# Performance work log

Hardware: AMD Instinct MI355X
Metric: run time of the kernel (lower is better)

The kernel has to match this reference:

```python
import jax, jax.numpy as jnp
import numpy as np

B, V, FIN, H = 200, 40, 16, 128
NSW = 12          # switch edges
NE = 40           # regular edges
M = NE + NSW      # 52 total edges
MLP_HID = 1024
OUT = M + V + NSW # 104


def _build_graph():
    rng = np.random.default_rng(0)
    pairs = set()
    while len(pairs) < M:
        i, j = map(int, rng.integers(0, V, 2))
        if i < j:
            pairs.add((i, j))
    pairs = sorted(pairs)
    reg = np.array(pairs[:NE], np.int64)   # (NE,2)
    sw = np.array(pairs[NE:], np.int64)    # (NSW,2) row-major sorted, matches torch.nonzero order
    edges = np.concatenate([reg, sw], 0)   # switch edges last, matching graph_topo layout
    A = np.zeros((V, M), np.float32)
    A[edges[:, 0], np.arange(M)] = 1.0
    A[edges[:, 1], np.arange(M)] = -1.0
    return reg, sw, A


def setup_inputs():
    key = jax.random.key(0)
    ks = jax.random.split(key, 16)
    reg, sw, A = _build_graph()
    ei = jnp.broadcast_to(jnp.asarray(reg.T)[None], (B, 2, NE))
    si = jnp.broadcast_to(jnp.asarray(sw.T)[None], (B, 2, NSW))

    def w(k, shp, fan):
        return jax.random.normal(k, shp, jnp.float32) / np.sqrt(fan)

    return {
        'x_mod': jax.random.normal(ks[0], (B, V, FIN), jnp.float32),
        'ei': ei, 'si': si, 'A_inc': jnp.asarray(A),
        'embed': w(ks[1], (2, FIN), 1.0),
        'WU0': w(ks[2], (FIN, H), FIN), 'WV0': w(ks[3], (FIN, H), FIN),
        'WA0': w(ks[4], (FIN, H), FIN), 'WB0': w(ks[5], (FIN, H), FIN),
        'WC0': w(ks[6], (FIN, H), FIN),
        'WU1': w(ks[7], (H, H), H), 'WV1': w(ks[8], (H, H), H),
        'WA1': w(ks[9], (H, H), H), 'WB1': w(ks[10], (H, H), H),
        'WC1': w(ks[11], (H, H), H),
        'W1': w(ks[12], ((NSW + V) * H, MLP_HID), (NSW + V) * H),
        'b1': jnp.zeros((MLP_HID,), jnp.float32),
        'W2': w(ks[13], (MLP_HID, OUT), MLP_HID),
        'b2': jnp.zeros((OUT,), jnp.float32),
    }


def _layer(x, s, adj, smask, WU, WV, WA, WB, WC, residual):
    Ux = x @ WU
    Vx = x @ WV
    # gate features over dense VxV switch grid: e_ij = A s_ij + B x_i + C x_j
    e = jnp.einsum('bijf,fh->bijh', s, WA) + (x @ WB)[:, :, None, :] + (x @ WC)[:, None, :, :]
    gates = jax.nn.sigmoid(e) * smask[..., None]
    msg_edges = jnp.einsum('bij,bjh->bih', adj, Vx)   # regular-edge aggregation
    msg_sw = jnp.einsum('bijh,bjh->bih', gates, Vx)   # gated switch aggregation
    xh = jax.nn.relu(Ux + msg_edges + msg_sw)
    sh = jax.nn.relu(e)
    if residual:
        xh = x + xh
        sh = s + sh
    return xh, sh


def reference(x_mod, ei, si, A_inc, embed, WU0, WV0, WA0, WB0, WC0,
              WU1, WV1, WA1, WB1, WC1, W1, b1, W2, b2):
    i_sw, j_sw = si[0, 0], si[0, 1]   # switch indices (shared across batch)
    i_e, j_e = ei[0, 0], ei[0, 1]
    S = jnp.zeros((V, V), bool).at[i_sw, j_sw].set(True)   # upper-tri switch mask
    smask = jnp.broadcast_to(S, (B, V, V)).astype(x_mod.dtype)
    s0 = embed[S.astype(jnp.int32)]                        # (V,V,FIN) edge embedding
    s = jnp.broadcast_to(s0[None], (B, V, V, FIN))
    adj1 = jnp.zeros((V, V), x_mod.dtype).at[i_e, j_e].set(1.0)
    adj = jnp.broadcast_to((adj1 + adj1.T)[None], (B, V, V))
    x, s = _layer(x_mod, s, adj, smask, WU0, WV0, WA0, WB0, WC0, residual=False)
    x, s = _layer(x, s, adj, smask, WU1, WV1, WA1, WB1, WC1, residual=True)
    switches = s[:, i_sw, j_sw, :]                         # (B,NSW,H) irregular gather (torch.nonzero path)
    mlp_in = jnp.concatenate([switches.reshape(B, -1), x.reshape(B, -1)], axis=1)
    out = jax.nn.relu(mlp_in @ W1 + b1) @ W2 + b2          # (B,OUT)
    p_switch = jax.nn.sigmoid(out[:, -NSW:])
    graph_topo = jnp.ones((B, M), out.dtype).at[:, M - NSW:].set(p_switch)
    v = out[:, M:M + V].at[:, 0].set(1.0)
    p_fc = graph_topo * out[:, :M]
    q_fc = graph_topo * (v @ A_inc)                        # per-edge voltage difference flow
    pg = x_mod[:, :, 0] + jnp.einsum('vm,bm->bv', A_inc, p_fc)  # power balance completion
    qg = x_mod[:, :, 1] + jnp.einsum('vm,bm->bv', A_inc, q_fc)
    z = jnp.concatenate([p_fc, v, graph_topo], axis=1)     # (B, 2M+V)
    zc = jnp.concatenate([q_fc, pg, qg], axis=1)           # (B, M+2V)
    return z, zc
```

## Files before the change

kernel.cpp:

```cpp
#include <hip/hip_runtime.h>
#include <math.h>

#define B       200
#define V       40
#define FIN     16
#define H       128
#define NSW     12
#define NE      40
#define M       52
#define MLP_HID 1024
#define OUTD    104
#define MLP_IN  6656
#define ZDIM    144
#define ZCDIM   132
#define NCH     13
#define X1LD    136
#define MAXD    16

typedef __attribute__((ext_vector_type(8))) short bf16x8;
typedef __attribute__((ext_vector_type(4))) float f32x4;

__device__ __forceinline__ float sigmoidf(float x) {
    return 1.0f / (1.0f + expf(-x));
}
__device__ __forceinline__ unsigned short f2b(float x) {
    unsigned int u = __float_as_uint(x);
    u += 0x7fffu + ((u >> 16) & 1u);
    return (unsigned short)(u >> 16);
}
__device__ __forceinline__ float b2f(unsigned short s) {
    return __uint_as_float(((unsigned int)s) << 16);
}

__global__ __launch_bounds__(256) void k_prep(
        const float* __restrict__ WU0, const float* __restrict__ WV0,
        const float* __restrict__ WB0, const float* __restrict__ WC0,
        const float* __restrict__ WU1, const float* __restrict__ WV1,
        const float* __restrict__ WB1, const float* __restrict__ WC1,
        const float* __restrict__ WA1, const float* __restrict__ W2,
        unsigned short* __restrict__ W0t, unsigned short* __restrict__ Wt640,
        unsigned short* __restrict__ W2t) {
    int bx = blockIdx.x, tid = threadIdx.x;
    if (bx < 64) {
        int o0 = bx * 2048 + tid * 8;
#pragma unroll
        for (int i = 0; i < 8; ++i) {
            int o = o0 + i; int col = o >> 10, k = o & 1023;
            W2t[o] = (col < OUTD) ? f2b(W2[(size_t)k * OUTD + col]) : (unsigned short)0;
        }
    } else if (bx < 104) {
        int o0 = (bx - 64) * 2048 + tid * 8;
#pragma unroll
        for (int i = 0; i < 8; ++i) {
            int o = o0 + i; int col = o >> 7, f = o & 127;
            int m = col >> 7, hh = col & 127;
            const float* Ws = (m == 0) ? WU1 : (m == 1) ? WV1 : (m == 2) ? WB1
                            : (m == 3) ? WC1 : WA1;
            Wt640[o] = f2b(Ws[f * H + hh]);
        }
    } else {
        int o0 = (bx - 104) * 2048 + tid * 8;
#pragma unroll
        for (int i = 0; i < 8; ++i) {
            int o = o0 + i; int col = o >> 5, k = o & 31;
            int m = col >> 7, hh = col & 127;
            const float* Ws = (m == 0) ? WU0 : (m == 1) ? WV0 : (m == 2) ? WB0 : WC0;
            W0t[o] = (k < FIN) ? f2b(Ws[k * H + hh]) : (unsigned short)0;
        }
    }
}

__global__ __launch_bounds__(512) void k_gnn(const float* __restrict__ x,
        const int* __restrict__ ei, const int* __restrict__ si,
        const float* __restrict__ embed, const float* __restrict__ WA0,
        const unsigned short* __restrict__ W0t,
        const unsigned short* __restrict__ Wt640,
        unsigned short* __restrict__ Abf) {
    int b = blockIdx.x, tid = threadIdx.x;
    __shared__ unsigned short xb[48 * 40];
    __shared__ unsigned short uvbc[V * 512];
    __shared__ unsigned short x1l[64 * X1LD];
    __shared__ float gL[NSW * H];
    __shared__ float sA1l[NSW * H];
    __shared__ int   nbr[V][MAXD];
    __shared__ int   deg[V];

    int h = tid & 127, sub = tid >> 7;
    int lane = tid & 63, wv = tid >> 6;
    int lr = lane & 15, lk = lane >> 4;
    int n0w = wv * 64;

    for (int o = tid; o < 48 * 32; o += 512) {
        int r = o >> 5, k = o & 31;
        float v = (r < V && k < FIN) ? x[(size_t)b * V * FIN + r * FIN + k] : 0.f;
        xb[r * 40 + k] = f2b(v);
    }
    if (tid < V) deg[tid] = 0;
    for (int o = tid; o < 12 * 128; o += 512) {
        int rr = o >> 7;
        int row = (rr < 8) ? 40 + rr : 60 + (rr - 8);
        x1l[row * X1LD + (o & 127)] = 0;
    }
    __syncthreads();

    if (tid < NE) {
        int i = ei[tid], j = ei[NE + tid];
        int p = atomicAdd(&deg[i], 1); if (p < MAXD) nbr[i][p] = j;
        int q = atomicAdd(&deg[j], 1); if (q < MAXD) nbr[j][q] = i;
    } else if (tid < NE + NSW) {
        int k = tid - NE;
        int i = si[k], j = si[NSW + k];
        int p = atomicAdd(&deg[i], 1); if (p < MAXD) nbr[i][p] = j | ((k + 1) << 8);
    }
    {
        f32x4 acc[3][4];
#pragma unroll
        for (int rf = 0; rf < 3; ++rf)
#pragma unroll
            for (int cf = 0; cf < 4; ++cf) acc[rf][cf] = (f32x4){0.f, 0.f, 0.f, 0.f};
        int kseg = lk * 8;
        bf16x8 a0 = *(const bf16x8*)&xb[lr * 40 + kseg];
        bf16x8 a1 = *(const bf16x8*)&xb[(16 + lr) * 40 + kseg];
        bf16x8 a2 = *(const bf16x8*)&xb[(32 + lr) * 40 + kseg];
#pragma unroll
        for (int cf = 0; cf < 4; ++cf) {
            bf16x8 bf = *(const bf16x8*)&W0t[(n0w + cf * 16 + lr) * 32 + kseg];
            acc[0][cf] = __builtin_amdgcn_mfma_f32_16x16x32_bf16(a0, bf, acc[0][cf], 0, 0, 0);
            acc[1][cf] = __builtin_amdgcn_mfma_f32_16x16x32_bf16(a1, bf, acc[1][cf], 0, 0, 0);
            acc[2][cf] = __builtin_amdgcn_mfma_f32_16x16x32_bf16(a2, bf, acc[2][cf], 0, 0, 0);
        }
#pragma unroll
        for (int rf = 0; rf < 3; ++rf)
#pragma unroll
            for (int cf = 0; cf < 4; ++cf)
#pragma unroll
                for (int r = 0; r < 4; ++r) {
                    int row = rf * 16 + lk * 4 + r;
                    if (row < V) uvbc[row * 512 + n0w + cf * 16 + lr] = f2b(acc[rf][cf][r]);
                }
    }
    __syncthreads();

    {
        float sA0 = 0.f;
#pragma unroll
        for (int f = 0; f < FIN; ++f) sA0 += embed[FIN + f] * WA0[f * H + h];
        for (int k = sub; k < NSW; k += 4) {
            int i = si[k], j = si[NSW + k];
            float e0 = sA0 + b2f(uvbc[i * 512 + 256 + h]) + b2f(uvbc[j * 512 + 384 + h]);
            gL[k * H + h] = sigmoidf(e0);
            x1l[(48 + k) * X1LD + h] = f2b(fmaxf(e0, 0.f));
        }
    }
    __syncthreads();

    for (int i = sub * 10; i < sub * 10 + 10; ++i) {
        float acc = b2f(uvbc[i * 512 + h]);
        int d = deg[i]; if (d > MAXD) d = MAXD;
        for (int p = 0; p < d; ++p) {
            int ent = nbr[i][p];
            float vv = b2f(uvbc[(ent & 255) * 512 + 128 + h]);
            int g = ent >> 8;
            if (g) vv *= gL[(g - 1) * H + h];
            acc += vv;
        }
        x1l[i * X1LD + h] = f2b(fmaxf(acc, 0.f));
    }
    __syncthreads();

    {
        f32x4 acc[3][4], accs = (f32x4){0.f, 0.f, 0.f, 0.f};
#pragma unroll
        for (int rf = 0; rf < 3; ++rf)
#pragma unroll
            for (int cf = 0; cf < 4; ++cf) acc[rf][cf] = (f32x4){0.f, 0.f, 0.f, 0.f};
#pragma unroll
        for (int kk = 0; kk < 4; ++kk) {
            int kseg = kk * 32 + lk * 8;
            bf16x8 a0 = *(const bf16x8*)&x1l[lr * X1LD + kseg];
            bf16x8 a1 = *(const bf16x8*)&x1l[(16 + lr) * X1LD + kseg];
            bf16x8 a2 = *(const bf16x8*)&x1l[(32 + lr) * X1LD + kseg];
            bf16x8 as = *(const bf16x8*)&x1l[(48 + lr) * X1LD + kseg];
#pragma unroll
            for (int cf = 0; cf < 4; ++cf) {
                bf16x8 bf = *(const bf16x8*)&Wt640[(size_t)(n0w + cf * 16 + lr) * H + kseg];
                acc[0][cf] = __builtin_amdgcn_mfma_f32_16x16x32_bf16(a0, bf, acc[0][cf], 0, 0, 0);
                acc[1][cf] = __builtin_amdgcn_mfma_f32_16x16x32_bf16(a1, bf, acc[1][cf], 0, 0, 0);
                acc[2][cf] = __builtin_amdgcn_mfma_f32_16x16x32_bf16(a2, bf, acc[2][cf], 0, 0, 0);
            }
            bf16x8 bs = *(const bf16x8*)&Wt640[(size_t)(512 + wv * 16 + lr) * H + kseg];
            accs = __builtin_amdgcn_mfma_f32_16x16x32_bf16(as, bs, accs, 0, 0, 0);
        }
#pragma unroll
        for (int rf = 0; rf < 3; ++rf)
#pragma unroll
            for (int cf = 0; cf < 4; ++cf)
#pragma unroll
                for (int r = 0; r < 4; ++r) {
                    int row = rf * 16 + lk * 4 + r;
                    if (row < V) uvbc[row * 512 + n0w + cf * 16 + lr] = f2b(acc[rf][cf][r]);
                }
#pragma unroll
        for (int r = 0; r < 4; ++r) {
            int sr = lk * 4 + r;
            if (sr < NSW) sA1l[sr * H + wv * 16 + lr] = accs[r];
        }
    }
    __syncthreads();

    for (int k = sub; k < NSW; k += 4) {
        int i = si[k], j = si[NSW + k];
        float e1 = sA1l[k * H + h] + b2f(uvbc[i * 512 + 256 + h]) + b2f(uvbc[j * 512 + 384 + h]);
        gL[k * H + h] = sigmoidf(e1);
        float s1 = b2f(x1l[(48 + k) * X1LD + h]);
        Abf[(size_t)b * MLP_IN + k * H + h] = f2b(s1 + fmaxf(e1, 0.f));
    }
    __syncthreads();

    for (int i = sub * 10; i < sub * 10 + 10; ++i) {
        float acc = b2f(uvbc[i * 512 + h]);
        int d = deg[i]; if (d > MAXD) d = MAXD;
        for (int p = 0; p < d; ++p) {
            int ent = nbr[i][p];
            float vv = b2f(uvbc[(ent & 255) * 512 + 128 + h]);
            int g = ent >> 8;
            if (g) vv *= gL[(g - 1) * H + h];
            acc += vv;
        }
        float x2 = b2f(x1l[i * X1LD + h]) + fmaxf(acc, 0.f);
        Abf[(size_t)b * MLP_IN + NSW * H + i * H + h] = f2b(x2);
    }
}

__global__ __launch_bounds__(256) void k_mlp(const unsigned short* __restrict__ A,
        const float* __restrict__ W1, float* __restrict__ partial) {
    const int NK = 16;
    int tid = threadIdx.x;
    int lane = tid & 63, wvv = tid >> 6;
    int wr = (wvv >> 1) * 32, wc = (wvv & 1) * 32;
    int n0 = blockIdx.x * 64, m0 = blockIdx.y * 64;
    int kbase = blockIdx.z * NK * 32;

    __shared__ __align__(16) unsigned short a_lds[64 * 40];
    __shared__ __align__(16) unsigned short b_lds[64 * 40];

    f32x4 acc00 = {0,0,0,0}, acc01 = {0,0,0,0}, acc10 = {0,0,0,0}, acc11 = {0,0,0,0};

    int srow = tid >> 2, sseg = tid & 3;
    const int4* gA = (const int4*)(A + (size_t)(m0 + srow) * MLP_IN + kbase + sseg * 8);
    int lwsA = srow * 40 + sseg * 8;

    int bcol = tid & 63, bkg = tid >> 6;
    const float* gW = W1 + (size_t)(kbase + bkg * 8) * MLP_HID + n0 + bcol;
    int lwsB = bcol * 40 + bkg * 8;

    int a_off = (wr + (lane & 15)) * 40 + (lane >> 4) * 8;
    int b_off = (wc + (lane & 15)) * 40 + (lane >> 4) * 8;

    int4 ra = gA[0];
    float rfv[8];
#pragma unroll
    for (int i = 0; i < 8; ++i) rfv[i] = gW[(size_t)i * MLP_HID];

    for (int kk = 0; kk < NK; ++kk) {
        *(int4*)&a_lds[lwsA] = ra;
        union { unsigned short us[8]; int4 v; } pk;
#pragma unroll
        for (int i = 0; i < 8; ++i) pk.us[i] = f2b(rfv[i]);
        *(int4*)&b_lds[lwsB] = pk.v;
        __syncthreads();
        if (kk + 1 < NK) {
            ra = gA[(kk + 1) * 4];
            const float* g2 = gW + (size_t)(kk + 1) * 32 * MLP_HID;
#pragma unroll
            for (int i = 0; i < 8; ++i) rfv[i] = g2[(size_t)i * MLP_HID];
        }
        bf16x8 a0 = *(const bf16x8*)&a_lds[a_off];
        bf16x8 a1 = *(const bf16x8*)&a_lds[a_off + 16 * 40];
        bf16x8 b0 = *(const bf16x8*)&b_lds[b_off];
        bf16x8 b1 = *(const bf16x8*)&b_lds[b_off + 16 * 40];
        acc00 = __builtin_amdgcn_mfma_f32_16x16x32_bf16(a0, b0, acc00, 0, 0, 0);
        acc01 = __builtin_amdgcn_mfma_f32_16x16x32_bf16(a0, b1, acc01, 0, 0, 0);
        acc10 = __builtin_amdgcn_mfma_f32_16x16x32_bf16(a1, b0, acc10, 0, 0, 0);
        acc11 = __builtin_amdgcn_mfma_f32_16x16x32_bf16(a1, b1, acc11, 0, 0, 0);
        __syncthreads();
    }

    int crow = (lane >> 4) * 4, ccol = lane & 15;
    int row0 = m0 + wr + crow, row1 = row0 + 16;
    int col0 = n0 + wc + ccol, col1 = col0 + 16;
    float* dst = partial + (size_t)blockIdx.z * 256 * MLP_HID;
#pragma unroll
    for (int r = 0; r < 4; ++r) {
        dst[(size_t)(row0 + r) * MLP_HID + col0] = acc00[r];
        dst[(size_t)(row0 + r) * MLP_HID + col1] = acc01[r];
        dst[(size_t)(row1 + r) * MLP_HID + col0] = acc10[r];
        dst[(size_t)(row1 + r) * MLP_HID + col1] = acc11[r];
    }
}

template<int MODE>
__global__ __launch_bounds__(256) void k_gemm(const unsigned short* __restrict__ A,
        const unsigned short* __restrict__ Bt, void* __restrict__ Cout,
        int K, int nk, int ldc) {
    int tid = threadIdx.x;
    int lane = tid & 63, wv = tid >> 6;
    int wr = (wv >> 1) * 32, wc = (wv & 1) * 32;
    int n0 = blockIdx.x * 64, m0 = blockIdx.y * 64;
    size_t kbase = (size_t)blockIdx.z * nk * 32;

    __shared__ __align__(16) unsigned short a_lds[64 * 40];
    __shared__ __align__(16) unsigned short b_lds[64 * 40];

    f32x4 acc00 = {0,0,0,0}, acc01 = {0,0,0,0}, acc10 = {0,0,0,0}, acc11 = {0,0,0,0};

    int srow = tid >> 2, sseg = tid & 3;
    const int4* gA = (const int4*)(A + (size_t)(m0 + srow) * K + kbase + sseg * 8);
    const int4* gB = (const int4*)(Bt + (size_t)(n0 + srow) * K + kbase + sseg * 8);
    int lws = srow * 40 + sseg * 8;

    int a_off = (wr + (lane & 15)) * 40 + (lane >> 4) * 8;
    int b_off = (wc + (lane & 15)) * 40 + (lane >> 4) * 8;

    int4 ra = gA[0], rb = gB[0];
    for (int kk = 0; kk < nk; ++kk) {
        *(int4*)&a_lds[lws] = ra;
        *(int4*)&b_lds[lws] = rb;
        __syncthreads();
        if (kk + 1 < nk) { ra = gA[(kk + 1) * 4]; rb = gB[(kk + 1) * 4]; }
        bf16x8 a0 = *(const bf16x8*)&a_lds[a_off];
        bf16x8 a1 = *(const bf16x8*)&a_lds[a_off + 16 * 40];
        bf16x8 b0 = *(const bf16x8*)&b_lds[b_off];
        bf16x8 b1 = *(const bf16x8*)&b_lds[b_off + 16 * 40];
        acc00 = __builtin_amdgcn_mfma_f32_16x16x32_bf16(a0, b0, acc00, 0, 0, 0);
        acc01 = __builtin_amdgcn_mfma_f32_16x16x32_bf16(a0, b1, acc01, 0, 0, 0);
        acc10 = __builtin_amdgcn_mfma_f32_16x16x32_bf16(a1, b0, acc10, 0, 0, 0);
        acc11 = __builtin_amdgcn_mfma_f32_16x16x32_bf16(a1, b1, acc11, 0, 0, 0);
        __syncthreads();
    }

    int crow = (lane >> 4) * 4, ccol = lane & 15;
    int row0 = m0 + wr + crow, row1 = row0 + 16;
    int col0 = n0 + wc + ccol, col1 = col0 + 16;
    float* dst = (float*)Cout + (size_t)blockIdx.z * (gridDim.y * 64) * ldc;
#pragma unroll
    for (int r = 0; r < 4; ++r) {
        dst[(size_t)(row0 + r) * ldc + col0] = acc00[r];
        dst[(size_t)(row0 + r) * ldc + col1] = acc01[r];
        dst[(size_t)(row1 + r) * ldc + col0] = acc10[r];
        dst[(size_t)(row1 + r) * ldc + col1] = acc11[r];
    }
}

__global__ void k_mred(const float* __restrict__ partial, const float* __restrict__ b1,
                       unsigned short* __restrict__ hiddenb) {
    int i = blockIdx.x * 256 + threadIdx.x;
    float s = b1[i & (MLP_HID - 1)];
#pragma unroll
    for (int z = 0; z < NCH; ++z) s += partial[(size_t)z * 256 * MLP_HID + i];
    hiddenb[i] = f2b(fmaxf(s, 0.f));
}

__global__ __launch_bounds__(128) void k_fin(const float* __restrict__ partial2,
        const float* __restrict__ b2, const float* __restrict__ A,
        const float* __restrict__ x_mod, float* __restrict__ outp) {
    int b = blockIdx.x;
    int tid = threadIdx.x;
    __shared__ float o[OUTD];
    __shared__ float gt[M], vv[V], pfc[M], qfc[M];

    if (tid < OUTD) {
        float s = b2[tid];
#pragma unroll
        for (int z = 0; z < 4; ++z) s += partial2[(size_t)z * 256 * 128 + b * 128 + tid];
        o[tid] = s;
    }
    __syncthreads();

    if (tid < M) {
        float g = (tid < M - NSW) ? 1.0f : sigmoidf(o[M + V + (tid - (M - NSW))]);
        gt[tid] = g;
        pfc[tid] = g * o[tid];
    }
    if (tid < V) vv[tid] = (tid == 0) ? 1.0f : o[M + tid];
    __syncthreads();

    if (tid < M) {
        float acc = 0.f;
        for (int x = 0; x < V; ++x) acc += vv[x] * A[x * M + tid];
        qfc[tid] = gt[tid] * acc;
    }
    __syncthreads();

    float* zb = outp + (size_t)b * ZDIM;
    if (tid < M) zb[tid] = pfc[tid];
    if (tid < V) zb[M + tid] = vv[tid];
    if (tid < M) zb[M + V + tid] = gt[tid];

    float* zcb = outp + (size_t)B * ZDIM + (size_t)b * ZCDIM;
    if (tid < M) zcb[tid] = qfc[tid];
    if (tid < V) {
        float accp = 0.f, accq = 0.f;
        for (int m = 0; m < M; ++m) {
            float a = A[tid * M + m];
            accp += a * pfc[m];
            accq += a * qfc[m];
        }
        zcb[M + tid]     = x_mod[(size_t)(b * V + tid) * FIN + 0] + accp;
        zcb[M + V + tid] = x_mod[(size_t)(b * V + tid) * FIN + 1] + accq;
    }
}

extern "C" void kernel_launch(void* const* d_in, const int* in_sizes, int n_in,
                              void* d_out, int out_size, void* d_ws, size_t ws_size,
                              hipStream_t stream) {
    const float* x_mod = (const float*)d_in[0];
    const int*   ei    = (const int*)d_in[1];
    const int*   si    = (const int*)d_in[2];
    const float* A     = (const float*)d_in[3];
    const float* embed = (const float*)d_in[4];
    const float* WU0   = (const float*)d_in[5];
    const float* WV0   = (const float*)d_in[6];
    const float* WA0   = (const float*)d_in[7];
    const float* WB0   = (const float*)d_in[8];
    const float* WC0   = (const float*)d_in[9];
    const float* WU1   = (const float*)d_in[10];
    const float* WV1   = (const float*)d_in[11];
    const float* WA1   = (const float*)d_in[12];
    const float* WB1   = (const float*)d_in[13];
    const float* WC1   = (const float*)d_in[14];
    const float* W1    = (const float*)d_in[15];
    const float* b1    = (const float*)d_in[16];
    const float* W2    = (const float*)d_in[17];
    const float* b2    = (const float*)d_in[18];
    float* out = (float*)d_out;

    char* ws = (char*)d_ws;
    unsigned short* W0t      = (unsigned short*)(ws + 0);
    unsigned short* Wt640    = (unsigned short*)(ws + 32768);
    unsigned short* W2t      = (unsigned short*)(ws + 196608);
    unsigned short* Abf      = (unsigned short*)(ws + 458752);
    float*          partialM = (float*)(ws + 3866624);
    unsigned short* hiddenb  = (unsigned short*)(ws + 17498112);
    float*          partial2 = (float*)(ws + 18022400);

    k_prep<<<112, 256, 0, stream>>>(WU0, WV0, WB0, WC0, WU1, WV1, WB1, WC1, WA1, W2,
                                    W0t, Wt640, W2t);
    k_gnn<<<B, 512, 0, stream>>>(x_mod, ei, si, embed, WA0, W0t, Wt640, Abf);
    k_mlp<<<dim3(16, 4, NCH), 256, 0, stream>>>(Abf, W1, partialM);
    k_mred<<<256 * MLP_HID / 256, 256, 0, stream>>>(partialM, b1, hiddenb);
    k_gemm<2><<<dim3(2, 4, 4), 256, 0, stream>>>(hiddenb, W2t, partial2, MLP_HID, 8, 128);
    k_fin<<<B, 128, 0, stream>>>(partial2, b2, A, x_mod, out);
}
```

Measured before the change: 56.48 us.

## Replace split-K partial buffers with atomic accumulation and fuse bias/ReLU into head GEMM

The MLP GEMM now accumulates split-K results directly into a zeroed fp32 hidden buffer with atomicAdd instead of writing per-chunk partials. This removes the separate reduction kernel. The second GEMM reads fp32 hidden values and W2 directly, applies bias and ReLU on load, and atomically accumulates into an output pre-filled with b2. The W2 transpose pass and two launches are gone. The MLP tile widens to 128 columns. The risks are atomic contention, non-deterministic summation order, and strided uncoalesced W2 loads in the head kernel.

```diff
diff --git a/kernel.cpp b/kernel.cpp
--- a/kernel.cpp
+++ b/kernel.cpp
@@ -37,19 +37,21 @@
         const float* __restrict__ WB0, const float* __restrict__ WC0,
         const float* __restrict__ WU1, const float* __restrict__ WV1,
         const float* __restrict__ WB1, const float* __restrict__ WC1,
-        const float* __restrict__ WA1, const float* __restrict__ W2,
+        const float* __restrict__ WA1, const float* __restrict__ b2,
         unsigned short* __restrict__ W0t, unsigned short* __restrict__ Wt640,
-        unsigned short* __restrict__ W2t) {
+        float* __restrict__ hiddenF, float* __restrict__ oF) {
     int bx = blockIdx.x, tid = threadIdx.x;
-    if (bx < 64) {
+    if (bx < 8) {
         int o0 = bx * 2048 + tid * 8;
 #pragma unroll
         for (int i = 0; i < 8; ++i) {
-            int o = o0 + i; int col = o >> 10, k = o & 1023;
-            W2t[o] = (col < OUTD) ? f2b(W2[(size_t)k * OUTD + col]) : (unsigned short)0;
-        }
-    } else if (bx < 104) {
-        int o0 = (bx - 64) * 2048 + tid * 8;
+            int o = o0 + i; int col = o >> 5, k = o & 31;
+            int m = col >> 7, hh = col & 127;
+            const float* Ws = (m == 0) ? WU0 : (m == 1) ? WV0 : (m == 2) ? WB0 : WC0;
+            W0t[o] = (k < FIN) ? f2b(Ws[k * H + hh]) : (unsigned short)0;
+        }
+    } else if (bx < 48) {
+        int o0 = (bx - 8) * 2048 + tid * 8;
 #pragma unroll
         for (int i = 0; i < 8; ++i) {
             int o = o0 + i; int col = o >> 7, f = o & 127;
@@ -58,14 +60,17 @@
                             : (m == 3) ? WC1 : WA1;
             Wt640[o] = f2b(Ws[f * H + hh]);
         }
+    } else if (bx < 80) {
+        float4 z = {0.f, 0.f, 0.f, 0.f};
+        float4* dst = (float4*)(hiddenF + (size_t)(bx - 48) * 8192) + tid;
+#pragma unroll
+        for (int i = 0; i < 8; ++i) dst[i * 256] = z;
     } else {
-        int o0 = (bx - 104) * 2048 + tid * 8;
-#pragma unroll
-        for (int i = 0; i < 8; ++i) {
-            int o = o0 + i; int col = o >> 5, k = o & 31;
-            int m = col >> 7, hh = col & 127;
-            const float* Ws = (m == 0) ? WU0 : (m == 1) ? WV0 : (m == 2) ? WB0 : WC0;
-            W0t[o] = (k < FIN) ? f2b(Ws[k * H + hh]) : (unsigned short)0;
+        int base = (bx - 80) * 8192 + tid * 32;
+#pragma unroll
+        for (int i = 0; i < 32; ++i) {
+            int o = base + i; int col = o & 127;
+            oF[o] = (col < OUTD) ? b2[col] : 0.f;
         }
     }
 }
@@ -233,148 +238,162 @@
 }
 
 __global__ __launch_bounds__(256) void k_mlp(const unsigned short* __restrict__ A,
-        const float* __restrict__ W1, float* __restrict__ partial) {
+        const float* __restrict__ W1, float* __restrict__ hiddenF) {
     const int NK = 16;
     int tid = threadIdx.x;
     int lane = tid & 63, wvv = tid >> 6;
-    int wr = (wvv >> 1) * 32, wc = (wvv & 1) * 32;
-    int n0 = blockIdx.x * 64, m0 = blockIdx.y * 64;
+    int wr = (wvv >> 1) * 32, wc = (wvv & 1) * 64;
+    int n0 = blockIdx.x * 128, m0 = blockIdx.y * 64;
     int kbase = blockIdx.z * NK * 32;
 
     __shared__ __align__(16) unsigned short a_lds[64 * 40];
-    __shared__ __align__(16) unsigned short b_lds[64 * 40];
-
-    f32x4 acc00 = {0,0,0,0}, acc01 = {0,0,0,0}, acc10 = {0,0,0,0}, acc11 = {0,0,0,0};
+    __shared__ __align__(16) unsigned short b_lds[128 * 40];
+
+    f32x4 acc[2][4];
+#pragma unroll
+    for (int r = 0; r < 2; ++r)
+#pragma unroll
+        for (int c = 0; c < 4; ++c) acc[r][c] = (f32x4){0.f, 0.f, 0.f, 0.f};
 
     int srow = tid >> 2, sseg = tid & 3;
     const int4* gA = (const int4*)(A + (size_t)(m0 + srow) * MLP_IN + kbase + sseg * 8);
     int lwsA = srow * 40 + sseg * 8;
 
-    int bcol = tid & 63, bkg = tid >> 6;
-    const float* gW = W1 + (size_t)(kbase + bkg * 8) * MLP_HID + n0 + bcol;
-    int lwsB = bcol * 40 + bkg * 8;
+    int bcol = tid & 127, bkg = tid >> 7;
+    const float* gW = W1 + (size_t)(kbase + bkg * 16) * MLP_HID + n0 + bcol;
+    int lwsB = bcol * 40 + bkg * 16;
 
     int a_off = (wr + (lane & 15)) * 40 + (lane >> 4) * 8;
     int b_off = (wc + (lane & 15)) * 40 + (lane >> 4) * 8;
 
     int4 ra = gA[0];
-    float rfv[8];
-#pragma unroll
-    for (int i = 0; i < 8; ++i) rfv[i] = gW[(size_t)i * MLP_HID];
+    float rf[16];
+#pragma unroll
+    for (int i = 0; i < 16; ++i) rf[i] = gW[(size_t)i * MLP_HID];
 
     for (int kk = 0; kk < NK; ++kk) {
         *(int4*)&a_lds[lwsA] = ra;
-        union { unsigned short us[8]; int4 v; } pk;
-#pragma unroll
-        for (int i = 0; i < 8; ++i) pk.us[i] = f2b(rfv[i]);
-        *(int4*)&b_lds[lwsB] = pk.v;
+        union { unsigned short us[16]; int4 v[2]; } pk;
+#pragma unroll
+        for (int i = 0; i < 16; ++i) pk.us[i] = f2b(rf[i]);
+        *(int4*)&b_lds[lwsB] = pk.v[0];
+        *(int4*)&b_lds[lwsB + 8] = pk.v[1];
         __syncthreads();
         if (kk + 1 < NK) {
             ra = gA[(kk + 1) * 4];
             const float* g2 = gW + (size_t)(kk + 1) * 32 * MLP_HID;
 #pragma unroll
-            for (int i = 0; i < 8; ++i) rfv[i] = g2[(size_t)i * MLP_HID];
+            for (int i = 0; i < 16; ++i) rf[i] = g2[(size_t)i * MLP_HID];
         }
         bf16x8 a0 = *(const bf16x8*)&a_lds[a_off];
         bf16x8 a1 = *(const bf16x8*)&a_lds[a_off + 16 * 40];
-        bf16x8 b0 = *(const bf16x8*)&b_lds[b_off];
-        bf16x8 b1 = *(const bf16x8*)&b_lds[b_off + 16 * 40];
-        acc00 = __builtin_amdgcn_mfma_f32_16x16x32_bf16(a0, b0, acc00, 0, 0, 0);
-        acc01 = __builtin_amdgcn_mfma_f32_16x16x32_bf16(a0, b1, acc01, 0, 0, 0);
-        acc10 = __builtin_amdgcn_mfma_f32_16x16x32_bf16(a1, b0, acc10, 0, 0, 0);
-        acc11 = __builtin_amdgcn_mfma_f32_16x16x32_bf16(a1, b1, acc11, 0, 0, 0);
+#pragma unroll
+        for (int c = 0; c < 4; ++c) {
+            bf16x8 bf = *(const bf16x8*)&b_lds[b_off + c * 16 * 40];
+            acc[0][c] = __builtin_amdgcn_mfma_f32_16x16x32_bf16(a0, bf, acc[0][c], 0, 0, 0);
+            acc[1][c] = __builtin_amdgcn_mfma_f32_16x16x32_bf16(a1, bf, acc[1][c], 0, 0, 0);
+        }
         __syncthreads();
     }
 
     int crow = (lane >> 4) * 4, ccol = lane & 15;
-    int row0 = m0 + wr + crow, row1 = row0 + 16;
-    int col0 = n0 + wc + ccol, col1 = col0 + 16;
-    float* dst = partial + (size_t)blockIdx.z * 256 * MLP_HID;
-#pragma unroll
-    for (int r = 0; r < 4; ++r) {
-        dst[(size_t)(row0 + r) * MLP_HID + col0] = acc00[r];
-        dst[(size_t)(row0 + r) * MLP_HID + col1] = acc01[r];
-        dst[(size_t)(row1 + r) * MLP_HID + col0] = acc10[r];
-        dst[(size_t)(row1 + r) * MLP_HID + col1] = acc11[r];
-    }
-}
-
-template<int MODE>
-__global__ __launch_bounds__(256) void k_gemm(const unsigned short* __restrict__ A,
-        const unsigned short* __restrict__ Bt, void* __restrict__ Cout,
-        int K, int nk, int ldc) {
+#pragma unroll
+    for (int r = 0; r < 2; ++r)
+#pragma unroll
+        for (int c = 0; c < 4; ++c) {
+            int row = m0 + wr + r * 16 + crow;
+            int col = n0 + wc + c * 16 + ccol;
+#pragma unroll
+            for (int e = 0; e < 4; ++e)
+                atomicAdd(&hiddenF[(size_t)(row + e) * MLP_HID + col], acc[r][c][e]);
+        }
+}
+
+__global__ __launch_bounds__(256) void k_head(const float* __restrict__ hiddenF,
+        const float* __restrict__ b1, const float* __restrict__ W2,
+        float* __restrict__ oF) {
+    const int NK = 8;
     int tid = threadIdx.x;
-    int lane = tid & 63, wv = tid >> 6;
-    int wr = (wv >> 1) * 32, wc = (wv & 1) * 32;
-    int n0 = blockIdx.x * 64, m0 = blockIdx.y * 64;
-    size_t kbase = (size_t)blockIdx.z * nk * 32;
+    int lane = tid & 63, wvv = tid >> 6;
+    int wr = (wvv >> 1) * 32, wc = (wvv & 1) * 64;
+    int m0 = blockIdx.y * 64;
+    int kbase = blockIdx.z * NK * 32;
 
     __shared__ __align__(16) unsigned short a_lds[64 * 40];
-    __shared__ __align__(16) unsigned short b_lds[64 * 40];
-
-    f32x4 acc00 = {0,0,0,0}, acc01 = {0,0,0,0}, acc10 = {0,0,0,0}, acc11 = {0,0,0,0};
+    __shared__ __align__(16) unsigned short b_lds[128 * 40];
+
+    f32x4 acc[2][4];
+#pragma unroll
+    for (int r = 0; r < 2; ++r)
+#pragma unroll
+        for (int c = 0; c < 4; ++c) acc[r][c] = (f32x4){0.f, 0.f, 0.f, 0.f};
 
     int srow = tid >> 2, sseg = tid & 3;
-    const int4* gA = (const int4*)(A + (size_t)(m0 + srow) * K + kbase + sseg * 8);
-    const int4* gB = (const int4*)(Bt + (size_t)(n0 + srow) * K + kbase + sseg * 8);
-    int lws = srow * 40 + sseg * 8;
+    const float* gH = hiddenF + (size_t)(m0 + srow) * MLP_HID + kbase + sseg * 8;
+    const float* gb = b1 + kbase + sseg * 8;
+    int lwsA = srow * 40 + sseg * 8;
+
+    int bcol = tid & 127, bkg = tid >> 7;
+    int lwsB = bcol * 40 + bkg * 16;
 
     int a_off = (wr + (lane & 15)) * 40 + (lane >> 4) * 8;
     int b_off = (wc + (lane & 15)) * 40 + (lane >> 4) * 8;
 
-    int4 ra = gA[0], rb = gB[0];
-    for (int kk = 0; kk < nk; ++kk) {
-        *(int4*)&a_lds[lws] = ra;
-        *(int4*)&b_lds[lws] = rb;
+    for (int kk = 0; kk < NK; ++kk) {
+        {
+            union { unsigned short us[8]; int4 v; } pa;
+#pragma unroll
+            for (int i = 0; i < 8; ++i) {
+                float v = gH[(size_t)kk * 32 + i] + gb[kk * 32 + i];
+                pa.us[i] = f2b(fmaxf(v, 0.f));
+            }
+            *(int4*)&a_lds[lwsA] = pa.v;
+        }
+        {
+            union { unsigned short us[16]; int4 v[2]; } pb;
+            int kb = kbase + kk * 32 + bkg * 16;
+#pragma unroll
+            for (int i = 0; i < 16; ++i) {
+                float v = (bcol < OUTD) ? W2[(size_t)(kb + i) * OUTD + bcol] : 0.f;
+                pb.us[i] = f2b(v);
+            }
+            *(int4*)&b_lds[lwsB] = pb.v[0];
+            *(int4*)&b_lds[lwsB + 8] = pb.v[1];
+        }
         __syncthreads();
-        if (kk + 1 < nk) { ra = gA[(kk + 1) * 4]; rb = gB[(kk + 1) * 4]; }
         bf16x8 a0 = *(const bf16x8*)&a_lds[a_off];
         bf16x8 a1 = *(const bf16x8*)&a_lds[a_off + 16 * 40];
-        bf16x8 b0 = *(const bf16x8*)&b_lds[b_off];
-        bf16x8 b1 = *(const bf16x8*)&b_lds[b_off + 16 * 40];
-        acc00 = __builtin_amdgcn_mfma_f32_16x16x32_bf16(a0, b0, acc00, 0, 0, 0);
-        acc01 = __builtin_amdgcn_mfma_f32_16x16x32_bf16(a0, b1, acc01, 0, 0, 0);
-        acc10 = __builtin_amdgcn_mfma_f32_16x16x32_bf16(a1, b0, acc10, 0, 0, 0);
-        acc11 = __builtin_amdgcn_mfma_f32_16x16x32_bf16(a1, b1, acc11, 0, 0, 0);
+#pragma unroll
+        for (int c = 0; c < 4; ++c) {
+            bf16x8 bf = *(const bf16x8*)&b_lds[b_off + c * 16 * 40];
+            acc[0][c] = __builtin_amdgcn_mfma_f32_16x16x32_bf16(a0, bf, acc[0][c], 0, 0, 0);
+            acc[1][c] = __builtin_amdgcn_mfma_f32_16x16x32_bf16(a1, bf, acc[1][c], 0, 0, 0);
+        }
         __syncthreads();
     }
 
     int crow = (lane >> 4) * 4, ccol = lane & 15;
-    int row0 = m0 + wr + crow, row1 = row0 + 16;
-    int col0 = n0 + wc + ccol, col1 = col0 + 16;
-    float* dst = (float*)Cout + (size_t)blockIdx.z * (gridDim.y * 64) * ldc;
-#pragma unroll
-    for (int r = 0; r < 4; ++r) {
-        dst[(size_t)(row0 + r) * ldc + col0] = acc00[r];
-        dst[(size_t)(row0 + r) * ldc + col1] = acc01[r];
-        dst[(size_t)(row1 + r) * ldc + col0] = acc10[r];
-        dst[(size_t)(row1 + r) * ldc + col1] = acc11[r];
-    }
-}
-
-__global__ void k_mred(const float* __restrict__ partial, const float* __restrict__ b1,
-                       unsigned short* __restrict__ hiddenb) {
-    int i = blockIdx.x * 256 + threadIdx.x;
-    float s = b1[i & (MLP_HID - 1)];
-#pragma unroll
-    for (int z = 0; z < NCH; ++z) s += partial[(size_t)z * 256 * MLP_HID + i];
-    hiddenb[i] = f2b(fmaxf(s, 0.f));
-}
-
-__global__ __launch_bounds__(128) void k_fin(const float* __restrict__ partial2,
-        const float* __restrict__ b2, const float* __restrict__ A,
-        const float* __restrict__ x_mod, float* __restrict__ outp) {
+#pragma unroll
+    for (int r = 0; r < 2; ++r)
+#pragma unroll
+        for (int c = 0; c < 4; ++c) {
+            int row = m0 + wr + r * 16 + crow;
+            int col = wc + c * 16 + ccol;
+#pragma unroll
+            for (int e = 0; e < 4; ++e)
+                atomicAdd(&oF[(size_t)(row + e) * 128 + col], acc[r][c][e]);
+        }
+}
+
+__global__ __launch_bounds__(128) void k_fin(const float* __restrict__ oF,
+        const float* __restrict__ A, const float* __restrict__ x_mod,
+        float* __restrict__ outp) {
     int b = blockIdx.x;
     int tid = threadIdx.x;
     __shared__ float o[OUTD];
     __shared__ float gt[M], vv[V], pfc[M], qfc[M];
 
-    if (tid < OUTD) {
-        float s = b2[tid];
-#pragma unroll
-        for (int z = 0; z < 4; ++z) s += partial2[(size_t)z * 256 * 128 + b * 128 + tid];
-        o[tid] = s;
-    }
+    if (tid < OUTD) o[tid] = oF[(size_t)b * 128 + tid];
     __syncthreads();
 
     if (tid < M) {
@@ -436,19 +455,16 @@
     float* out = (float*)d_out;
 
     char* ws = (char*)d_ws;
-    unsigned short* W0t      = (unsigned short*)(ws + 0);
-    unsigned short* Wt640    = (unsigned short*)(ws + 32768);
-    unsigned short* W2t      = (unsigned short*)(ws + 196608);
-    unsigned short* Abf      = (unsigned short*)(ws + 458752);
-    float*          partialM = (float*)(ws + 3866624);
-    unsigned short* hiddenb  = (unsigned short*)(ws + 17498112);
-    float*          partial2 = (float*)(ws + 18022400);
-
-    k_prep<<<112, 256, 0, stream>>>(WU0, WV0, WB0, WC0, WU1, WV1, WB1, WC1, WA1, W2,
-                                    W0t, Wt640, W2t);
+    unsigned short* W0t     = (unsigned short*)(ws + 0);
+    unsigned short* Wt640   = (unsigned short*)(ws + 32768);
+    unsigned short* Abf     = (unsigned short*)(ws + 196608);
+    float*          hiddenF = (float*)(ws + 3604480);
+    float*          oF      = (float*)(ws + 4653056);
+
+    k_prep<<<84, 256, 0, stream>>>(WU0, WV0, WB0, WC0, WU1, WV1, WB1, WC1, WA1, b2,
+                                   W0t, Wt640, hiddenF, oF);
     k_gnn<<<B, 512, 0, stream>>>(x_mod, ei, si, embed, WA0, W0t, Wt640, Abf);
-    k_mlp<<<dim3(16, 4, NCH), 256, 0, stream>>>(Abf, W1, partialM);
-    k_mred<<<256 * MLP_HID / 256, 256, 0, stream>>>(partialM, b1, hiddenb);
-    k_gemm<2><<<dim3(2, 4, 4), 256, 0, stream>>>(hiddenb, W2t, partial2, MLP_HID, 8, 128);
-    k_fin<<<B, 128, 0, stream>>>(partial2, b2, A, x_mod, out);
-}
+    k_mlp<<<dim3(8, 4, NCH), 256, 0, stream>>>(Abf, W1, hiddenF);
+    k_head<<<dim3(1, 4, 4), 256, 0, stream>>>(hiddenF, b1, W2, oF);
+    k_fin<<<B, 128, 0, stream>>>(oF, A, x_mod, out);
+}
```

New measurement: 70.89 us. +25.5%, slower.

## Cover all 256 rows per MLP block so W1 is read and converted once

Applied to the files above, without the earlier changes.

The first MLP GEMM kernel now has each block handle the full 256-row M dimension instead of a 64-row slice. Each wave owns 64 rows and accumulates a 4x4 grid of MFMA tiles. Previously four blocks along M each re-read and re-converted the same fp32 W1 tile to bf16. The grid shrinks from 16x4x13 to 16x1x13 (208 blocks), which cuts redundant W1 traffic but reduces parallelism, raises register use (64 accumulator floats), and grows LDS per block.

```diff
diff --git a/kernel.cpp b/kernel.cpp
--- a/kernel.cpp
+++ b/kernel.cpp
@@ -237,66 +237,81 @@
     const int NK = 16;
     int tid = threadIdx.x;
     int lane = tid & 63, wvv = tid >> 6;
-    int wr = (wvv >> 1) * 32, wc = (wvv & 1) * 32;
-    int n0 = blockIdx.x * 64, m0 = blockIdx.y * 64;
+    int n0 = blockIdx.x * 64;
     int kbase = blockIdx.z * NK * 32;
 
-    __shared__ __align__(16) unsigned short a_lds[64 * 40];
+    __shared__ __align__(16) unsigned short a_lds[256 * 40];
     __shared__ __align__(16) unsigned short b_lds[64 * 40];
 
-    f32x4 acc00 = {0,0,0,0}, acc01 = {0,0,0,0}, acc10 = {0,0,0,0}, acc11 = {0,0,0,0};
+    f32x4 acc[4][4];
+#pragma unroll
+    for (int rf = 0; rf < 4; ++rf)
+#pragma unroll
+        for (int cf = 0; cf < 4; ++cf) acc[rf][cf] = (f32x4){0.f, 0.f, 0.f, 0.f};
 
     int srow = tid >> 2, sseg = tid & 3;
-    const int4* gA = (const int4*)(A + (size_t)(m0 + srow) * MLP_IN + kbase + sseg * 8);
+    const unsigned short* gA = A + (size_t)srow * MLP_IN + kbase + sseg * 8;
     int lwsA = srow * 40 + sseg * 8;
 
     int bcol = tid & 63, bkg = tid >> 6;
     const float* gW = W1 + (size_t)(kbase + bkg * 8) * MLP_HID + n0 + bcol;
     int lwsB = bcol * 40 + bkg * 8;
 
-    int a_off = (wr + (lane & 15)) * 40 + (lane >> 4) * 8;
-    int b_off = (wc + (lane & 15)) * 40 + (lane >> 4) * 8;
-
-    int4 ra = gA[0];
+    int lr = lane & 15, lk = lane >> 4;
+    int a_off = (wvv * 64 + lr) * 40 + lk * 8;
+    int b_off = lr * 40 + lk * 8;
+
+    int4 ra[4];
     float rfv[8];
 #pragma unroll
+    for (int g = 0; g < 4; ++g)
+        ra[g] = *(const int4*)(gA + (size_t)g * 64 * MLP_IN);
+#pragma unroll
     for (int i = 0; i < 8; ++i) rfv[i] = gW[(size_t)i * MLP_HID];
 
     for (int kk = 0; kk < NK; ++kk) {
-        *(int4*)&a_lds[lwsA] = ra;
-        union { unsigned short us[8]; int4 v; } pk;
-#pragma unroll
-        for (int i = 0; i < 8; ++i) pk.us[i] = f2b(rfv[i]);
-        *(int4*)&b_lds[lwsB] = pk.v;
+#pragma unroll
+        for (int g = 0; g < 4; ++g)
+            *(int4*)&a_lds[lwsA + g * 64 * 40] = ra[g];
+        {
+            union { unsigned short us[8]; int4 v; } pk;
+#pragma unroll
+            for (int i = 0; i < 8; ++i) pk.us[i] = f2b(rfv[i]);
+            *(int4*)&b_lds[lwsB] = pk.v;
+        }
         __syncthreads();
         if (kk + 1 < NK) {
-            ra = gA[(kk + 1) * 4];
+#pragma unroll
+            for (int g = 0; g < 4; ++g)
+                ra[g] = *(const int4*)(gA + (size_t)g * 64 * MLP_IN + (kk + 1) * 32);
             const float* g2 = gW + (size_t)(kk + 1) * 32 * MLP_HID;
 #pragma unroll
             for (int i = 0; i < 8; ++i) rfv[i] = g2[(size_t)i * MLP_HID];
         }
-        bf16x8 a0 = *(const bf16x8*)&a_lds[a_off];
-        bf16x8 a1 = *(const bf16x8*)&a_lds[a_off + 16 * 40];
-        bf16x8 b0 = *(const bf16x8*)&b_lds[b_off];
-        bf16x8 b1 = *(const bf16x8*)&b_lds[b_off + 16 * 40];
-        acc00 = __builtin_amdgcn_mfma_f32_16x16x32_bf16(a0, b0, acc00, 0, 0, 0);
-        acc01 = __builtin_amdgcn_mfma_f32_16x16x32_bf16(a0, b1, acc01, 0, 0, 0);
-        acc10 = __builtin_amdgcn_mfma_f32_16x16x32_bf16(a1, b0, acc10, 0, 0, 0);
-        acc11 = __builtin_amdgcn_mfma_f32_16x16x32_bf16(a1, b1, acc11, 0, 0, 0);
+        bf16x8 af[4], bf[4];
+#pragma unroll
+        for (int rf = 0; rf < 4; ++rf) af[rf] = *(const bf16x8*)&a_lds[a_off + rf * 16 * 40];
+#pragma unroll
+        for (int cf = 0; cf < 4; ++cf) bf[cf] = *(const bf16x8*)&b_lds[b_off + cf * 16 * 40];
+#pragma unroll
+        for (int rf = 0; rf < 4; ++rf)
+#pragma unroll
+            for (int cf = 0; cf < 4; ++cf)
+                acc[rf][cf] = __builtin_amdgcn_mfma_f32_16x16x32_bf16(af[rf], bf[cf], acc[rf][cf], 0, 0, 0);
         __syncthreads();
     }
 
-    int crow = (lane >> 4) * 4, ccol = lane & 15;
-    int row0 = m0 + wr + crow, row1 = row0 + 16;
-    int col0 = n0 + wc + ccol, col1 = col0 + 16;
     float* dst = partial + (size_t)blockIdx.z * 256 * MLP_HID;
 #pragma unroll
-    for (int r = 0; r < 4; ++r) {
-        dst[(size_t)(row0 + r) * MLP_HID + col0] = acc00[r];
-        dst[(size_t)(row0 + r) * MLP_HID + col1] = acc01[r];
-        dst[(size_t)(row1 + r) * MLP_HID + col0] = acc10[r];
-        dst[(size_t)(row1 + r) * MLP_HID + col1] = acc11[r];
-    }
+    for (int rf = 0; rf < 4; ++rf)
+#pragma unroll
+        for (int cf = 0; cf < 4; ++cf) {
+            int row = wvv * 64 + rf * 16 + lk * 4;
+            int col = n0 + cf * 16 + lr;
+#pragma unroll
+            for (int e = 0; e < 4; ++e)
+                dst[(size_t)(row + e) * MLP_HID + col] = acc[rf][cf][e];
+        }
 }
 
 template<int MODE>
@@ -447,7 +462,7 @@
     k_prep<<<112, 256, 0, stream>>>(WU0, WV0, WB0, WC0, WU1, WV1, WB1, WC1, WA1, W2,
                                     W0t, Wt640, W2t);
     k_gnn<<<B, 512, 0, stream>>>(x_mod, ei, si, embed, WA0, W0t, Wt640, Abf);
-    k_mlp<<<dim3(16, 4, NCH), 256, 0, stream>>>(Abf, W1, partialM);
+    k_mlp<<<dim3(16, 1, NCH), 256, 0, stream>>>(Abf, W1, partialM);
     k_mred<<<256 * MLP_HID / 256, 256, 0, stream>>>(partialM, b1, hiddenb);
     k_gemm<2><<<dim3(2, 4, 4), 256, 0, stream>>>(hiddenb, W2t, partial2, MLP_HID, 8, 128);
     k_fin<<<B, 128, 0, stream>>>(partial2, b2, A, x_mod, out);
```

After: 67.94 us. +20.3%, slower.
